# Optimization experiments

Hardware: AMD Instinct MI355X
Metric: run time of the kernel (lower is better)

## Reference

```python
import jax, jax.numpy as jnp
import numpy as np

REL_DIM = 1024
NUM_HEADS = 16
HEAD_DIM = REL_DIM // NUM_HEADS
REL_EMB_DIM = 256
B, K = 32, 512
SCALE = 1.0 / float(np.sqrt(HEAD_DIM))


def setup_inputs() -> dict:
    key = jax.random.key(0)
    ks = jax.random.split(key, 7)
    s = 1.0 / float(np.sqrt(REL_DIM))
    return {
        "h_R": jax.random.normal(ks[0], (B, K, REL_DIM), dtype=jnp.float32),
        "R": jax.random.normal(ks[1], (K, REL_EMB_DIM), dtype=jnp.float32),
        "W_q": jax.random.normal(ks[2], (REL_DIM, REL_DIM), dtype=jnp.float32) * s,
        "W_k": jax.random.normal(ks[3], (REL_DIM, REL_DIM), dtype=jnp.float32) * s,
        "W_v": jax.random.normal(ks[4], (REL_DIM, REL_DIM), dtype=jnp.float32) * s,
        "W_o": jax.random.normal(ks[5], (REL_DIM, REL_DIM), dtype=jnp.float32) * s,
        "w_sim": jax.random.normal(ks[6], (NUM_HEADS,), dtype=jnp.float32) * 0.1,
    }


def reference(h_R, R, W_q, W_k, W_v, W_o, w_sim):
    Bb, Kk, _ = h_R.shape
    H, D = NUM_HEADS, HEAD_DIM
    # torch Linear: x @ W.T ; then split heads -> (B, H, K, D)
    def proj(x, W):
        return jnp.einsum('bkd,ed->bke', x, W).reshape(Bb, Kk, H, D).transpose(0, 2, 1, 3)
    q = proj(h_R, W_q)
    k = proj(h_R, W_k)
    v = proj(h_R, W_v)
    attn = jnp.einsum('bhqd,bhkd->bhqk', q, k) * SCALE
    # cosine-similarity bias (batch-independent): (H, K, K)
    R_norm = R / jnp.maximum(jnp.linalg.norm(R, axis=-1, keepdims=True), 1e-12)
    sim = R_norm @ R_norm.T  # (K, K)
    bias = w_sim[:, None, None] * sim[None]  # (H, K, K)
    attn = attn + bias[None]
    alpha = jax.nn.softmax(attn, axis=-1)
    out = jnp.einsum('bhqk,bhkd->bhqd', alpha, v)
    out = out.transpose(0, 2, 1, 3).reshape(Bb, Kk, H * D)
    return jnp.einsum('bkd,ed->bke', out, W_o)
```

## Files before the change

kernel.cpp:

```cpp
#include <hip/hip_runtime.h>

#define SEQK 512
#define NH 16
#define HD 64
#define RD 1024
#define BBATCH 32
#define QK_SCALE 0.125f
#define LOG2E 1.4426950408889634f

typedef unsigned short u16;
typedef unsigned int u32;
using bf16x8 = __attribute__((ext_vector_type(8))) short;
using f32x4  = __attribute__((ext_vector_type(4))) float;
using f32x16 = __attribute__((ext_vector_type(16))) float;

__device__ __forceinline__ u16 f2bf(float f) {
  unsigned u = __float_as_uint(f);
  u += 0x7FFFu + ((u >> 16) & 1u);
  return (u16)(u >> 16);
}
__device__ __forceinline__ float bf2f(u16 v) {
  return __uint_as_float(((unsigned)v) << 16);
}
__device__ __forceinline__ float fexp2(float x) {
  float r;
  asm("v_exp_f32 %0, %1" : "=v"(r) : "v"(x));
  return r;
}
__device__ __forceinline__ u32 pkbf(float lo, float hi) {
  u32 r;
  asm("v_cvt_pk_bf16_f32 %0, %1, %2" : "=v"(r) : "v"(lo), "v"(hi));
  return r;
}
__device__ __forceinline__ void plswap(u32& a, u32& b) {
#if __has_builtin(__builtin_amdgcn_permlane32_swap)
  typedef int v2i __attribute__((ext_vector_type(2)));
  v2i r = __builtin_amdgcn_permlane32_swap((int)a, (int)b, false, false);
  a = (u32)r[0]; b = (u32)r[1];
#else
  asm volatile("v_permlane32_swap_b32 %0, %1" : "+v"(a), "+v"(b));
#endif
}

__device__ __forceinline__ void async_cp16(const void* g, void* l) {
  __builtin_amdgcn_global_load_lds(
      (__attribute__((address_space(1))) void*)(void*)g,
      (__attribute__((address_space(3))) void*)l,
      16, 0, 0);
}

__global__ void convert_kernel(const float* __restrict__ hR,
                               const float* __restrict__ Wq, const float* __restrict__ Wk,
                               const float* __restrict__ Wv, const float* __restrict__ Wo,
                               u16* __restrict__ hR16,
                               u16* __restrict__ Wq16, u16* __restrict__ Wk16,
                               u16* __restrict__ Wv16, u16* __restrict__ Wo16) {
  size_t i4 = (size_t)blockIdx.x * blockDim.x + threadIdx.x;
  size_t e = i4 * 4;
  const float* src; u16* dst; size_t off;
  if (e < 16777216u) { src = hR; dst = hR16; off = e; }
  else {
    size_t r = e - 16777216u;
    int w = (int)(r >> 20);
    off = r & 1048575u;
    src = (w == 0 ? Wq : w == 1 ? Wk : w == 2 ? Wv : Wo);
    dst = (w == 0 ? Wq16 : w == 1 ? Wk16 : w == 2 ? Wv16 : Wo16);
  }
  float4 v = *(const float4*)(src + off);
  ushort4 o;
  o.x = f2bf(v.x); o.y = f2bf(v.y); o.z = f2bf(v.z); o.w = f2bf(v.w);
  *(ushort4*)(dst + off) = o;
}

__global__ void rnorm_kernel(const float* __restrict__ R, float* __restrict__ Rn) {
  int row = blockIdx.x;
  int lane = threadIdx.x;
  float4 v = *(const float4*)(R + (size_t)row * 256 + lane * 4);
  float ss = v.x * v.x + v.y * v.y + v.z * v.z + v.w * v.w;
  for (int off = 32; off; off >>= 1) ss += __shfl_xor(ss, off);
  float s = 1.0f / fmaxf(sqrtf(ss), 1e-12f);
  float4 o = {v.x * s, v.y * s, v.z * s, v.w * s};
  *(float4*)(Rn + (size_t)row * 256 + lane * 4) = o;
}

__global__ void sim_kernel(const float* __restrict__ Rn, u16* __restrict__ sim16) {
  __shared__ float Rl[16 * 256];
  int i0 = blockIdx.x * 16;
  int t = threadIdx.x;
  #pragma unroll
  for (int i = 0; i < 4; i++) {
    int f = t + i * 256;
    *(float4*)&Rl[f * 4] = *(const float4*)(Rn + (size_t)i0 * 256 + f * 4);
  }
  __syncthreads();
  for (int jj = 0; jj < 2; jj++) {
    int j = jj * 256 + t;
    float acc[16];
    #pragma unroll
    for (int i = 0; i < 16; i++) acc[i] = 0.f;
    for (int c = 0; c < 64; c++) {
      float4 rv = *(const float4*)(Rn + (size_t)j * 256 + c * 4);
      #pragma unroll
      for (int i = 0; i < 16; i++) {
        float4 a = *(const float4*)&Rl[i * 256 + c * 4];
        acc[i] += a.x * rv.x + a.y * rv.y + a.z * rv.z + a.w * rv.w;
      }
    }
    #pragma unroll
    for (int i = 0; i < 16; i++) sim16[(size_t)(i0 + i) * 512 + j] = f2bf(acc[i]);
  }
}

#define GEMM_PHASE(AB, BB, MH, NH, STAGE, WAITSTMT) {                         \
    bf16x8 af[4][2], bfv[2][2];                                               \
    _Pragma("unroll") for (int mi2 = 0; mi2 < 4; mi2++) {                     \
      int r = wm * 128 + ((MH) * 4 + mi2) * 16 + lr;                          \
      int sw = r & 7;                                                         \
      _Pragma("unroll") for (int ks = 0; ks < 2; ks++)                        \
        af[mi2][ks] = *(const bf16x8*)&(AB)[r * 64 + ((ks * 4 + qd) ^ sw) * 8]; \
    }                                                                         \
    _Pragma("unroll") for (int ni2 = 0; ni2 < 2; ni2++) {                     \
      int r = wn * 64 + ((NH) * 2 + ni2) * 16 + lr;                           \
      int sw = r & 7;                                                         \
      _Pragma("unroll") for (int ks = 0; ks < 2; ks++)                        \
        bfv[ni2][ks] = *(const bf16x8*)&(BB)[r * 64 + ((ks * 4 + qd) ^ sw) * 8]; \
    }                                                                         \
    STAGE;                                                                    \
    __builtin_amdgcn_sched_barrier(0);                                        \
    __builtin_amdgcn_s_barrier();                                             \
    __builtin_amdgcn_sched_barrier(0);                                        \
    __builtin_amdgcn_s_setprio(1);                                            \
    _Pragma("unroll") for (int mi2 = 0; mi2 < 4; mi2++)                       \
      _Pragma("unroll") for (int ni2 = 0; ni2 < 2; ni2++)                     \
        _Pragma("unroll") for (int ks = 0; ks < 2; ks++)                      \
          acc[(MH) * 4 + mi2][(NH) * 2 + ni2] =                               \
              __builtin_amdgcn_mfma_f32_16x16x32_bf16(                        \
                  af[mi2][ks], bfv[ni2][ks],                                  \
                  acc[(MH) * 4 + mi2][(NH) * 2 + ni2], 0, 0, 0);              \
    __builtin_amdgcn_s_setprio(0);                                            \
    WAITSTMT;                                                                 \
    __builtin_amdgcn_sched_barrier(0);                                        \
    __builtin_amdgcn_s_barrier();                                             \
  }

template <int MODE>
__global__ __launch_bounds__(512, 2)
void gemm_kernel(const u16* __restrict__ A,
                 const u16* __restrict__ B0, const u16* __restrict__ B1,
                 const u16* __restrict__ B2,
                 u16* __restrict__ q16, u16* __restrict__ k16, u16* __restrict__ v16,
                 float* __restrict__ outF) {
  __shared__ u16 smem[65536];
  u16* const As0 = smem;
  u16* const As1 = smem + 16384;
  u16* const Bs0 = smem + 32768;
  u16* const Bs1 = smem + 49152;

  int tid = threadIdx.x;
  int wave = tid >> 6, lane = tid & 63;
  int wm = wave >> 2, wn = wave & 3;
  int lr = lane & 15, qd = lane >> 4;
  int mb = blockIdx.x * 256;
  int ny = blockIdx.y;

  const u16* Bmat;
  int nbase;
  if (MODE == 0) {
    int wsel = ny >> 2;
    Bmat = (wsel == 0 ? B0 : wsel == 1 ? B1 : B2);
    nbase = (ny & 3) * 256;
  } else {
    Bmat = B0;
    nbase = ny * 256;
  }
  const u16* Ag = A + (size_t)mb * 1024;
  const u16* Bg = Bmat + (size_t)nbase * 1024;

  auto stageA_ = [&](u16* dst, const u16* gsrc, int half) {
    int blk = ((wave < 4) ? 0 : 2) + half;
    int ws = wave & 3;
    #pragma unroll
    for (int jj = 0; jj < 2; jj++) {
      int rbase = blk * 64 + ws * 16 + jj * 8;
      int row = rbase + (lane >> 3);
      int c8 = (lane & 7) ^ (row & 7);
      async_cp16(gsrc + (size_t)row * 1024 + c8 * 8, dst + rbase * 64);
    }
  };
  auto stageB_ = [&](u16* dst, const u16* gsrc, int half) {
    int st = wave >> 1, sub = wave & 1;
    #pragma unroll
    for (int jj = 0; jj < 2; jj++) {
      int rbase = st * 64 + half * 32 + sub * 16 + jj * 8;
      int row = rbase + (lane >> 3);
      int c8 = (lane & 7) ^ (row & 7);
      async_cp16(gsrc + (size_t)row * 1024 + c8 * 8, dst + rbase * 64);
    }
  };

  f32x4 acc[8][4];
  #pragma unroll
  for (int i = 0; i < 8; i++)
    #pragma unroll
    for (int j = 0; j < 4; j++) acc[i][j] = f32x4{0.f, 0.f, 0.f, 0.f};

  stageA_(As0, Ag, 0);
  stageB_(Bs0, Bg, 0);
  stageA_(As0, Ag, 1);
  stageB_(Bs0, Bg, 1);
  stageA_(As1, Ag + 64, 0);
  stageB_(Bs1, Bg + 64, 0);
  asm volatile("s_waitcnt vmcnt(4)" ::: "memory");
  __builtin_amdgcn_sched_barrier(0);
  __builtin_amdgcn_s_barrier();

  #pragma unroll 1
  for (int i = 0; i < 8; i++) {
    int t1 = 2 * i + 1;
    bool more = (i < 7);
    const u16* Ag1 = Ag + t1 * 64;
    const u16* Bg1 = Bg + t1 * 64;
    const u16* Ag2 = Ag + (t1 + 1) * 64;
    const u16* Bg2 = Bg + (t1 + 1) * 64;
    const u16* Ag3 = Ag + (t1 + 2) * 64;
    const u16* Bg3 = Bg + (t1 + 2) * 64;

    GEMM_PHASE(As0, Bs0, 0, 0, { stageA_(As1, Ag1, 1); }, {});
    GEMM_PHASE(As0, Bs0, 0, 1, { stageB_(Bs1, Bg1, 1); }, {});
    GEMM_PHASE(As0, Bs0, 1, 0, { if (more) stageA_(As0, Ag2, 0); }, {});
    GEMM_PHASE(As0, Bs0, 1, 1, { if (more) stageB_(Bs0, Bg2, 0); },
               { if (more) asm volatile("s_waitcnt vmcnt(4)" ::: "memory");
                 else      asm volatile("s_waitcnt vmcnt(0)" ::: "memory"); });
    GEMM_PHASE(As1, Bs1, 0, 0, { if (more) stageA_(As0, Ag2, 1); }, {});
    GEMM_PHASE(As1, Bs1, 0, 1, { if (more) stageB_(Bs0, Bg2, 1); }, {});
    GEMM_PHASE(As1, Bs1, 1, 0, { if (more) stageA_(As1, Ag3, 0); }, {});
    GEMM_PHASE(As1, Bs1, 1, 1, { if (more) stageB_(Bs1, Bg3, 0); },
               { if (more) asm volatile("s_waitcnt vmcnt(4)" ::: "memory"); });
  }

  if (MODE == 0) {
    int wsel = ny >> 2;
    u16* dst = (wsel == 0 ? q16 : wsel == 1 ? k16 : v16);
    float scl = (wsel == 0) ? QK_SCALE * LOG2E : 1.0f;
    #pragma unroll
    for (int mi = 0; mi < 8; mi++) {
      int m = mb + wm * 128 + mi * 16 + qd * 4;
      int b = m >> 9, kk = m & 511;
      #pragma unroll
      for (int ni = 0; ni < 4; ni++) {
        int n = nbase + wn * 64 + ni * 16 + lr;
        int h = n >> 6, d = n & 63;
        u16* p = dst + ((size_t)(b * 16 + h) * 512 + kk) * 64 + d;
        #pragma unroll
        for (int r = 0; r < 4; r++) p[(size_t)r * 64] = f2bf(acc[mi][ni][r] * scl);
      }
    }
  } else {
    #pragma unroll
    for (int mi = 0; mi < 8; mi++) {
      int m = mb + wm * 128 + mi * 16 + qd * 4;
      #pragma unroll
      for (int ni = 0; ni < 4; ni++) {
        int n = nbase + wn * 64 + ni * 16 + lr;
        #pragma unroll
        for (int r = 0; r < 4; r++) outF[(size_t)(m + r) * 1024 + n] = acc[mi][ni][r];
      }
    }
  }
}

__global__ void vtrans_kernel(const u16* __restrict__ v16, u16* __restrict__ vt16) {
  __shared__ u16 tile[64 * 72];
  int kt = blockIdx.x;
  int bh = blockIdx.y;
  int t = threadIdx.x;
  const u16* src = v16 + ((size_t)bh * 512 + kt * 64) * 64;
  #pragma unroll
  for (int j = 0; j < 2; j++) {
    int linear = j * 2048 + t * 8;
    int kr = linear >> 6, d0 = linear & 63;
    bf16x8 vv = *(const bf16x8*)(src + (size_t)kr * 64 + d0);
    #pragma unroll
    for (int e = 0; e < 8; e++) tile[kr * 72 + d0 + e] = (u16)vv[e];
  }
  __syncthreads();
  #pragma unroll
  for (int j = 0; j < 2; j++) {
    int linear = j * 2048 + t * 8;
    int dr = linear >> 6, k0 = linear & 63;
    bf16x8 ov;
    #pragma unroll
    for (int e = 0; e < 8; e++) ov[e] = (short)tile[(k0 + e) * 72 + dr];
    *(bf16x8*)(vt16 + ((size_t)bh * 64 + dr) * 512 + kt * 64 + k0) = ov;
  }
}

__global__ __launch_bounds__(256, 3)
void attn_kernel(const u16* __restrict__ q16, const u16* __restrict__ k16,
                 const u16* __restrict__ vt16, const u16* __restrict__ sim16,
                 const float* __restrict__ wsim, u16* __restrict__ attn16) {
  __shared__ u16 smem[16384];

  int id = blockIdx.x;
  int xcd = id & 7;
  int j = id >> 3;
  int qt = j & 3;
  int bh = xcd * 64 + (j >> 2);
  int b = bh >> 4, h = bh & 15;

  int tid = threadIdx.x;
  int wave = tid >> 6, lane = tid & 63;
  int l31 = lane & 31, hi = lane >> 5;
  int qb = qt * 128 + wave * 32;

  const u16* qp = q16 + ((size_t)bh * 512 + qb + l31) * 64 + hi * 8;
  bf16x8 aq[4];
  #pragma unroll
  for (int ds = 0; ds < 4; ds++) aq[ds] = *(const bf16x8*)(qp + ds * 16);

  float ws = wsim[h] * LOG2E;

  f32x16 o[2];
  #pragma unroll
  for (int dt = 0; dt < 2; dt++)
    #pragma unroll
    for (int r = 0; r < 16; r++) o[dt][r] = 0.f;
  float m_run = -1e30f, l_run = 0.f;

  const u16* kbase = k16 + (size_t)bh * 512 * 64;
  const u16* vbase = vt16 + (size_t)bh * 64 * 512;

  auto stage = [&](int nb, int ck) {
    int k0 = ck * 64;
    u16* kd = smem + nb * 4096;
    u16* vd = smem + 8192 + nb * 4096;
    #pragma unroll
    for (int it = 0; it < 2; it++) {
      int idx = it * 256 + wave * 64 + lane;
      int r = idx >> 3, c8 = idx & 7;
      async_cp16(kbase + (size_t)(k0 + r) * 64 + ((c8 ^ (r & 7)) << 3),
                 kd + (it * 256 + wave * 64) * 8);
    }
    #pragma unroll
    for (int it = 0; it < 2; it++) {
      int idx = it * 256 + wave * 64 + lane;
      int dr = idx >> 3, c8 = idx & 7;
      async_cp16(vbase + (size_t)dr * 512 + k0 + ((c8 ^ (dr & 7)) << 3),
                 vd + (it * 256 + wave * 64) * 8);
    }
  };

  stage(0, 0);
  __syncthreads();

  int cur = 0;
  for (int ck = 0; ck < 8; ck++) {
    int k0 = ck * 64;

    uint2 braw[8];
    #pragma unroll
    for (int kb = 0; kb < 2; kb++)
      #pragma unroll
      for (int g = 0; g < 4; g++)
        braw[kb * 4 + g] = *(const uint2*)(sim16 + (size_t)(qb + l31) * 512 +
                                           k0 + kb * 32 + g * 8 + hi * 4);
    __builtin_amdgcn_sched_barrier(0);
    if (ck < 7) stage(cur ^ 1, ck + 1);

    const u16* Kc = smem + cur * 4096;
    const u16* Vc = smem + 8192 + cur * 4096;

    f32x16 s[2];
    __builtin_amdgcn_s_setprio(1);
    #pragma unroll
    for (int kb = 0; kb < 2; kb++) {
      f32x16 acc;
      #pragma unroll
      for (int r = 0; r < 16; r++) {
        u32 w = ((r >> 1) & 1) ? braw[kb * 4 + (r >> 2)].y
                               : braw[kb * 4 + (r >> 2)].x;
        acc[r] = ws * __uint_as_float((r & 1) ? (w & 0xFFFF0000u) : (w << 16));
      }
      int koff = kb * 32 + l31;
      #pragma unroll
      for (int ds = 0; ds < 4; ds++) {
        bf16x8 kf = *(const bf16x8*)&Kc[koff * 64 + (((ds * 2 + hi) ^ (koff & 7)) << 3)];
        acc = __builtin_amdgcn_mfma_f32_32x32x16_bf16(kf, aq[ds], acc, 0, 0, 0);
      }
      s[kb] = acc;
    }
    __builtin_amdgcn_s_setprio(0);

    float v8[8];
    #pragma unroll
    for (int i = 0; i < 8; i++)
      v8[i] = fmaxf(fmaxf(s[0][i], s[0][i + 8]), fmaxf(s[1][i], s[1][i + 8]));
    float m_in = fmaxf(fmaxf(fmaxf(v8[0], v8[1]), fmaxf(v8[2], v8[3])),
                       fmaxf(fmaxf(v8[4], v8[5]), fmaxf(v8[6], v8[7])));
    u32 xa = __float_as_uint(m_in), xb = __float_as_uint(m_in);
    plswap(xa, xb);
    float m_tile = fmaxf(__uint_as_float(xa), __uint_as_float(xb));
    float mnew = fmaxf(m_run, m_tile);
    float alpha = fexp2(m_run - mnew);
    m_run = mnew;

    float c0 = 0.f, c1 = 0.f, c2 = 0.f, c3 = 0.f;
    #pragma unroll
    for (int kb = 0; kb < 2; kb++)
      #pragma unroll
      for (int i = 0; i < 16; i++) {
        float e = fexp2(s[kb][i] - mnew);
        s[kb][i] = e;
        if ((i & 3) == 0) c0 += e; else if ((i & 3) == 1) c1 += e;
        else if ((i & 3) == 2) c2 += e; else c3 += e;
      }
    float cs = (c0 + c1) + (c2 + c3);
    u32 ya = __float_as_uint(cs), yb = __float_as_uint(cs);
    plswap(ya, yb);
    float cs_tot = __uint_as_float(ya) + __uint_as_float(yb);
    l_run = l_run * alpha + cs_tot;

    #pragma unroll
    for (int dt = 0; dt < 2; dt++) o[dt] *= alpha;

    __builtin_amdgcn_s_setprio(1);
    #pragma unroll
    for (int ks = 0; ks < 4; ks++) {
      int kb = ks >> 1, j4 = (ks & 1) * 8;
      u32 a0 = pkbf(s[kb][j4 + 0], s[kb][j4 + 1]);
      u32 a1 = pkbf(s[kb][j4 + 2], s[kb][j4 + 3]);
      u32 b0 = pkbf(s[kb][j4 + 4], s[kb][j4 + 5]);
      u32 b1 = pkbf(s[kb][j4 + 6], s[kb][j4 + 7]);
      plswap(a0, b0);
      plswap(a1, b1);
      union { u32 w[4]; bf16x8 v; } U;
      U.w[0] = a0; U.w[1] = a1; U.w[2] = b0; U.w[3] = b1;
      #pragma unroll
      for (int dt = 0; dt < 2; dt++) {
        int dr = dt * 32 + l31;
        bf16x8 vf = *(const bf16x8*)&Vc[dr * 64 + (((ks * 2 + hi) ^ (dr & 7)) << 3)];
        o[dt] = __builtin_amdgcn_mfma_f32_32x32x16_bf16(vf, U.v, o[dt], 0, 0, 0);
      }
    }
    __builtin_amdgcn_s_setprio(0);

    __syncthreads();
    cur ^= 1;
  }

  float linv = 1.0f / l_run;
  u16* Ow = smem + wave * 2304;
  #pragma unroll
  for (int dt = 0; dt < 2; dt++)
    #pragma unroll
    for (int g = 0; g < 4; g++) {
      u32 w0 = pkbf(o[dt][4 * g + 0] * linv, o[dt][4 * g + 1] * linv);
      u32 w1 = pkbf(o[dt][4 * g + 2] * linv, o[dt][4 * g + 3] * linv);
      uint2 pr; pr.x = w0; pr.y = w1;
      *(uint2*)&Ow[l31 * 72 + dt * 32 + g * 8 + hi * 4] = pr;
    }
  #pragma unroll
  for (int i = 0; i < 4; i++) {
    int idx = i * 64 + lane;
    int row = idx >> 3, seg = idx & 7;
    bf16x8 val = *(const bf16x8*)&Ow[row * 72 + seg * 8];
    *(bf16x8*)(attn16 + ((size_t)b * 512 + qb + row) * 1024 + h * 64 + seg * 8) = val;
  }
}

extern "C" void kernel_launch(void* const* d_in, const int* in_sizes, int n_in,
                              void* d_out, int out_size, void* d_ws, size_t ws_size,
                              hipStream_t stream) {
  const float* hR  = (const float*)d_in[0];
  const float* R   = (const float*)d_in[1];
  const float* Wq  = (const float*)d_in[2];
  const float* Wk  = (const float*)d_in[3];
  const float* Wv  = (const float*)d_in[4];
  const float* Wo  = (const float*)d_in[5];
  const float* wsm = (const float*)d_in[6];
  float* out = (float*)d_out;

  const size_t NE = 16777216;
  u16* ws16   = (u16*)d_ws;
  u16* hR16   = ws16;
  u16* attn16 = ws16;
  u16* q16    = ws16 + NE;
  u16* k16    = ws16 + 2 * NE;
  u16* v16    = ws16 + 3 * NE;
  u16* vt16   = ws16 + 4 * NE;
  u16* Wq16   = ws16 + 5 * NE;
  u16* Wk16   = Wq16 + 1048576;
  u16* Wv16   = Wk16 + 1048576;
  u16* Wo16   = Wv16 + 1048576;
  u16* sim16  = Wo16 + 1048576;
  float* Rn   = (float*)(sim16 + 262144);

  convert_kernel<<<20480, 256, 0, stream>>>(hR, Wq, Wk, Wv, Wo,
                                            hR16, Wq16, Wk16, Wv16, Wo16);
  rnorm_kernel<<<512, 64, 0, stream>>>(R, Rn);
  sim_kernel<<<32, 256, 0, stream>>>(Rn, sim16);
  gemm_kernel<0><<<dim3(64, 12), 512, 0, stream>>>(hR16, Wq16, Wk16, Wv16,
                                                   q16, k16, v16, nullptr);
  vtrans_kernel<<<dim3(8, 512), 256, 0, stream>>>(v16, vt16);
  attn_kernel<<<2048, 256, 0, stream>>>(q16, k16, vt16, sim16, wsm, attn16);
  gemm_kernel<1><<<dim3(64, 4), 512, 0, stream>>>(attn16, Wo16, nullptr, nullptr,
                                                  nullptr, nullptr, nullptr, out);
}
```

Measured before the change: 432.7 us.

## Merge GEMM phases into two per tile, reusing B fragments across M halves

Restructures the bf16 MFMA GEMM main loop from four quarter-phases per k-tile into two half-phases. The first phase loads all four B fragments and keeps them in registers, and the second phase reuses them for the other M half. This cuts LDS reads of B and halves the number of block barriers per tile. In exchange it needs more registers for the held B fragments, issues two staging loads per phase, and has fewer points where global loads interleave with compute, which may hurt occupancy or overlap.

```diff
diff --git a/kernel.cpp b/kernel.cpp
--- a/kernel.cpp
+++ b/kernel.cpp
@@ -111,19 +111,19 @@
   }
 }
 
-#define GEMM_PHASE(AB, BB, MH, NH, STAGE, WAITSTMT) {                         \
-    bf16x8 af[4][2], bfv[2][2];                                               \
+#define GEMM_PHASE_E(AB, BB, STAGE, WAITSTMT) {                               \
+    bf16x8 af[4][2];                                                          \
     _Pragma("unroll") for (int mi2 = 0; mi2 < 4; mi2++) {                     \
-      int r = wm * 128 + ((MH) * 4 + mi2) * 16 + lr;                          \
+      int r = wm * 128 + mi2 * 16 + lr;                                       \
       int sw = r & 7;                                                         \
       _Pragma("unroll") for (int ks = 0; ks < 2; ks++)                        \
         af[mi2][ks] = *(const bf16x8*)&(AB)[r * 64 + ((ks * 4 + qd) ^ sw) * 8]; \
     }                                                                         \
-    _Pragma("unroll") for (int ni2 = 0; ni2 < 2; ni2++) {                     \
-      int r = wn * 64 + ((NH) * 2 + ni2) * 16 + lr;                           \
+    _Pragma("unroll") for (int nj = 0; nj < 4; nj++) {                        \
+      int r = wn * 64 + nj * 16 + lr;                                         \
       int sw = r & 7;                                                         \
       _Pragma("unroll") for (int ks = 0; ks < 2; ks++)                        \
-        bfv[ni2][ks] = *(const bf16x8*)&(BB)[r * 64 + ((ks * 4 + qd) ^ sw) * 8]; \
+        bq[nj][ks] = *(const bf16x8*)&(BB)[r * 64 + ((ks * 4 + qd) ^ sw) * 8]; \
     }                                                                         \
     STAGE;                                                                    \
     __builtin_amdgcn_sched_barrier(0);                                        \
@@ -131,12 +131,34 @@
     __builtin_amdgcn_sched_barrier(0);                                        \
     __builtin_amdgcn_s_setprio(1);                                            \
     _Pragma("unroll") for (int mi2 = 0; mi2 < 4; mi2++)                       \
-      _Pragma("unroll") for (int ni2 = 0; ni2 < 2; ni2++)                     \
+      _Pragma("unroll") for (int nj = 0; nj < 4; nj++)                        \
         _Pragma("unroll") for (int ks = 0; ks < 2; ks++)                      \
-          acc[(MH) * 4 + mi2][(NH) * 2 + ni2] =                               \
-              __builtin_amdgcn_mfma_f32_16x16x32_bf16(                        \
-                  af[mi2][ks], bfv[ni2][ks],                                  \
-                  acc[(MH) * 4 + mi2][(NH) * 2 + ni2], 0, 0, 0);              \
+          acc[mi2][nj] = __builtin_amdgcn_mfma_f32_16x16x32_bf16(             \
+              af[mi2][ks], bq[nj][ks], acc[mi2][nj], 0, 0, 0);                \
+    __builtin_amdgcn_s_setprio(0);                                            \
+    WAITSTMT;                                                                 \
+    __builtin_amdgcn_sched_barrier(0);                                        \
+    __builtin_amdgcn_s_barrier();                                             \
+  }
+
+#define GEMM_PHASE_O(AB, STAGE, WAITSTMT) {                                   \
+    bf16x8 af[4][2];                                                          \
+    _Pragma("unroll") for (int mi2 = 0; mi2 < 4; mi2++) {                     \
+      int r = wm * 128 + 64 + mi2 * 16 + lr;                                  \
+      int sw = r & 7;                                                         \
+      _Pragma("unroll") for (int ks = 0; ks < 2; ks++)                        \
+        af[mi2][ks] = *(const bf16x8*)&(AB)[r * 64 + ((ks * 4 + qd) ^ sw) * 8]; \
+    }                                                                         \
+    STAGE;                                                                    \
+    __builtin_amdgcn_sched_barrier(0);                                        \
+    __builtin_amdgcn_s_barrier();                                             \
+    __builtin_amdgcn_sched_barrier(0);                                        \
+    __builtin_amdgcn_s_setprio(1);                                            \
+    _Pragma("unroll") for (int mi2 = 0; mi2 < 4; mi2++)                       \
+      _Pragma("unroll") for (int nj = 0; nj < 4; nj++)                        \
+        _Pragma("unroll") for (int ks = 0; ks < 2; ks++)                      \
+          acc[4 + mi2][nj] = __builtin_amdgcn_mfma_f32_16x16x32_bf16(         \
+              af[mi2][ks], bq[nj][ks], acc[4 + mi2][nj], 0, 0, 0);            \
     __builtin_amdgcn_s_setprio(0);                                            \
     WAITSTMT;                                                                 \
     __builtin_amdgcn_sched_barrier(0);                                        \
@@ -225,17 +247,19 @@
     const u16* Ag3 = Ag + (t1 + 2) * 64;
     const u16* Bg3 = Bg + (t1 + 2) * 64;
 
-    GEMM_PHASE(As0, Bs0, 0, 0, { stageA_(As1, Ag1, 1); }, {});
-    GEMM_PHASE(As0, Bs0, 0, 1, { stageB_(Bs1, Bg1, 1); }, {});
-    GEMM_PHASE(As0, Bs0, 1, 0, { if (more) stageA_(As0, Ag2, 0); }, {});
-    GEMM_PHASE(As0, Bs0, 1, 1, { if (more) stageB_(Bs0, Bg2, 0); },
-               { if (more) asm volatile("s_waitcnt vmcnt(4)" ::: "memory");
-                 else      asm volatile("s_waitcnt vmcnt(0)" ::: "memory"); });
-    GEMM_PHASE(As1, Bs1, 0, 0, { if (more) stageA_(As0, Ag2, 1); }, {});
-    GEMM_PHASE(As1, Bs1, 0, 1, { if (more) stageB_(Bs0, Bg2, 1); }, {});
-    GEMM_PHASE(As1, Bs1, 1, 0, { if (more) stageA_(As1, Ag3, 0); }, {});
-    GEMM_PHASE(As1, Bs1, 1, 1, { if (more) stageB_(Bs1, Bg3, 0); },
-               { if (more) asm volatile("s_waitcnt vmcnt(4)" ::: "memory"); });
+    bf16x8 bq[4][2];
+
+    GEMM_PHASE_E(As0, Bs0,
+                 { stageA_(As1, Ag1, 1); stageB_(Bs1, Bg1, 1); }, {});
+    GEMM_PHASE_O(As0,
+                 { if (more) { stageA_(As0, Ag2, 0); stageB_(Bs0, Bg2, 0); } },
+                 { if (more) asm volatile("s_waitcnt vmcnt(4)" ::: "memory");
+                   else      asm volatile("s_waitcnt vmcnt(0)" ::: "memory"); });
+    GEMM_PHASE_E(As1, Bs1,
+                 { if (more) { stageA_(As0, Ag2, 1); stageB_(Bs0, Bg2, 1); } }, {});
+    GEMM_PHASE_O(As1,
+                 { if (more) { stageA_(As1, Ag3, 0); stageB_(Bs1, Bg3, 0); } },
+                 { if (more) asm volatile("s_waitcnt vmcnt(4)" ::: "memory"); });
   }
 
   if (MODE == 0) {
```

Result: faster. 415.5 us (-4.0%).
